# Performance work log

Measured on AMD Instinct MI355X. Metric: run time of the kernel, lower is better.

The kernel has to match this reference:

```python
import jax, jax.numpy as jnp
import numpy as np

N_LAYERS = 24  # number of recurrent applications of the shared HashLinear


def setup_inputs() -> dict:
    key = jax.random.key(0)
    ks = jax.random.split(key, 9)
    B, D_IN, N, N_OUT = 1024, 784, 4096, 10
    s_in = 1.0 / np.sqrt(D_IN)
    s_h = 1.0 / np.sqrt(N)
    x = jax.random.normal(ks[0], (B, D_IN), jnp.float32)
    # nn.Linear(prod(input_dim), 2*n_units)
    W_in = jax.random.uniform(ks[1], (2 * N, D_IN), jnp.float32, -s_in, s_in)
    b_in = jax.random.uniform(ks[2], (2 * N,), jnp.float32, -s_in, s_in)
    # HashLinear(n_units, n_units, period=1, 'hash'): learnable +/-1 context key + shared linear
    key_sp = jnp.where(jax.random.bernoulli(ks[3], 0.5, (1, N)), 1.0, -1.0).astype(jnp.float32)
    W_sp = jax.random.uniform(ks[4], (N, N), jnp.float32, -s_h, s_h)
    b_sp = jax.random.uniform(ks[5], (N,), jnp.float32, -s_h, s_h)
    # HashLinear(n_units, 10, period=1, 'hash')
    key_f = jnp.where(jax.random.bernoulli(ks[6], 0.5, (1, N)), 1.0, -1.0).astype(jnp.float32)
    W_f = jax.random.uniform(ks[7], (N_OUT, N), jnp.float32, -s_h, s_h)
    b_f = jax.random.uniform(ks[8], (N_OUT,), jnp.float32, -s_h, s_h)
    return {"x": x, "W_in": W_in, "b_in": b_in, "key_sp": key_sp, "W_sp": W_sp,
            "b_sp": b_sp, "key_f": key_f, "W_f": W_f, "b_f": b_f, "time": 0}


def _hash_linear(xa, xb, o, W, b):
    # Superposition HashLinear: same shared weight applied to both streams,
    # each modulated by the +/-1 context key o ([n_in]).
    ya = (xa * o) @ W.T + b
    yb = (xb * o) @ W.T + b
    return ya, yb


def reference(x, W_in, b_in, key_sp, W_sp, b_sp, key_f, W_f, b_f, time):
    N = W_sp.shape[0]
    r = x @ W_in.T + b_in                 # [B, 2N]
    r_a, r_b = r[:, :N], r[:, N:]         # torch.split(r, n_units, 1)
    pre0 = r_a
    r_a, r_b = jax.nn.relu(r_a), jax.nn.relu(r_b)
    o = key_sp[time % key_sp.shape[0]]    # period=1, time=0 in the module

    def step(carry, _):
        a, b2 = carry
        ya, yb = _hash_linear(a, b2, o, W_sp, b_sp)
        return (jax.nn.relu(ya), jax.nn.relu(yb)), ya  # collect preactivation r_a

    (r_a, r_b), pres = jax.lax.scan(step, (r_a, r_b), None, length=N_LAYERS)
    of = key_f[time % key_f.shape[0]]
    out_a, out_b = _hash_linear(r_a, r_b, of, W_f, b_f)  # [B,10], [B,10]
    preactivations = jnp.concatenate([pre0[None], pres], axis=0)  # [N_LAYERS+1, B, N]
    return (out_a, out_b, preactivations)
```

## Files before the change

kernel.cpp:

```cpp
#include <hip/hip_runtime.h>
#include <hip/hip_bf16.h>
#include <stdint.h>

typedef __bf16 bf16x8 __attribute__((ext_vector_type(8)));
typedef float  f32x4  __attribute__((ext_vector_type(4)));
typedef unsigned short ushort8v __attribute__((ext_vector_type(8)));

#define NH      4096
#define MB      1024
#define M2      2048
#define DIN     784
#define KPAD    832
#define N_IN    8192
#define NLAYERS 24
#define NOUT    10

#define ASL     (128 * 64)
#define SLOT    (2 * ASL)

__device__ __forceinline__ unsigned short f2bf(float x) {
  union { float f; unsigned u; } v; v.f = x;
  unsigned r = v.u + 0x7FFFu + ((v.u >> 16) & 1u);
  return (unsigned short)(r >> 16);
}
__device__ __forceinline__ float bf2f(unsigned short u) {
  union { unsigned u; float f; } v; v.u = ((unsigned)u) << 16; return v.f;
}

__device__ __forceinline__ void async16(const void* g, void* l) {
  __builtin_amdgcn_global_load_lds(
      (const __attribute__((address_space(1))) void*)g,
      (__attribute__((address_space(3))) void*)l, 16, 0, 0);
}

__global__ void k_conv_wsp(const float* __restrict__ W, const float* __restrict__ o,
                           unsigned short* __restrict__ out) {
  size_t i = ((size_t)blockIdx.x * blockDim.x + threadIdx.x) * 4;
  if (i >= (size_t)NH * NH) return;
  float4 w = *reinterpret_cast<const float4*>(W + i);
  int k = (int)(i & (NH - 1));
  float4 ov = *reinterpret_cast<const float4*>(o + k);
  ushort4 r;
  r.x = f2bf(w.x * ov.x); r.y = f2bf(w.y * ov.y);
  r.z = f2bf(w.z * ov.z); r.w = f2bf(w.w * ov.w);
  *reinterpret_cast<ushort4*>(out + i) = r;
}

__global__ void k_conv_pad2(const float* __restrict__ Win, const float* __restrict__ x,
                            unsigned short* __restrict__ Win_bf,
                            unsigned short* __restrict__ X_bf) {
  size_t i = (size_t)blockIdx.x * blockDim.x + threadIdx.x;
  if (i >= (size_t)(N_IN + MB) * KPAD) return;
  int r = (int)(i / KPAD), c = (int)(i % KPAD);
  if (r < N_IN) Win_bf[i] = (c < DIN) ? f2bf(Win[(size_t)r * DIN + c]) : (unsigned short)0;
  else {
    int rr = r - N_IN;
    X_bf[(size_t)rr * KPAD + c] = (c < DIN) ? f2bf(x[(size_t)rr * DIN + c]) : (unsigned short)0;
  }
}

__device__ __forceinline__ void gemm_core(
    const unsigned short* __restrict__ Ag, const unsigned short* __restrict__ Bg,
    int K, int bm, int bn, unsigned short* lds, f32x4 acc[4][4])
{
  const int t    = threadIdx.x;
  const int lane = t & 63;
  const int wave = t >> 6;
  const int wm   = wave >> 1;
  const int wn   = wave & 1;
  const int l15  = lane & 15;
  const int lkb  = (lane >> 4) * 16;

  const int srow = t >> 3;
  const int sb   = ((t & 7) * 16) ^ ((srow & 7) << 4);
  const unsigned aG0 = (unsigned)((bm + srow) * K + (sb >> 1));
  const unsigned bG0 = (unsigned)((bn + srow) * K + (sb >> 1));

  auto STAGE = [&](int bufIdx, int k0) {
    unsigned short* s = lds + bufIdx * SLOT;
#pragma unroll
    for (int j = 0; j < 4; ++j)
      async16(Ag + aG0 + (unsigned)(j * 32 * K + k0), s + t * 8 + j * 2048);
#pragma unroll
    for (int j = 0; j < 4; ++j)
      async16(Bg + bG0 + (unsigned)(j * 32 * K + k0), s + ASL + t * 8 + j * 2048);
  };

  int aRd[2][4], bRd[2][4];
#pragma unroll
  for (int kk = 0; kk < 2; ++kk)
#pragma unroll
    for (int i = 0; i < 4; ++i) {
      const int ra = wm * 64 + i * 16 + l15;
      aRd[kk][i] = (ra * 128 + ((kk * 64 + lkb) ^ ((ra & 7) << 4))) >> 1;
      const int rb = wn * 64 + i * 16 + l15;
      bRd[kk][i] = (rb * 128 + ((kk * 64 + lkb) ^ ((rb & 7) << 4))) >> 1;
    }

  const int nt = K >> 6;
  STAGE(0, 0);
  asm volatile("s_waitcnt vmcnt(0)" ::: "memory");
  __builtin_amdgcn_s_barrier();

  int buf = 0;
  for (int kt = 0; kt < nt; ++kt) {
    if (kt + 1 < nt) STAGE(buf ^ 1, (kt + 1) << 6);
    const unsigned short* base = lds + buf * SLOT;
    __builtin_amdgcn_s_setprio(1);
#pragma unroll
    for (int kk = 0; kk < 2; ++kk) {
      bf16x8 a[4], b[4];
#pragma unroll
      for (int i = 0; i < 4; ++i) a[i] = *reinterpret_cast<const bf16x8*>(base + aRd[kk][i]);
#pragma unroll
      for (int i = 0; i < 4; ++i) b[i] = *reinterpret_cast<const bf16x8*>(base + ASL + bRd[kk][i]);
#pragma unroll
      for (int mi = 0; mi < 4; ++mi)
#pragma unroll
        for (int ni = 0; ni < 4; ++ni)
          acc[mi][ni] = __builtin_amdgcn_mfma_f32_16x16x32_bf16(a[mi], b[ni], acc[mi][ni], 0, 0, 0);
    }
    __builtin_amdgcn_s_setprio(0);
    if (kt + 1 < nt) {
      asm volatile("s_waitcnt vmcnt(0)" ::: "memory");
      __builtin_amdgcn_s_barrier();
    }
    buf ^= 1;
  }
}

__global__ __launch_bounds__(256, 2) void k_gemm_layer(
    const unsigned short* __restrict__ A, const unsigned short* __restrict__ W,
    const float* __restrict__ bias, float* __restrict__ preact,
    unsigned short* __restrict__ Anext)
{
  __shared__ __align__(16) unsigned short lds[2 * SLOT];
  const int bid = blockIdx.x;
  const int xcd = bid & 7;
  const int idx = bid >> 3;
  const int bm  = (idx >> 2) * 128;
  const int bn  = (xcd * 4 + (idx & 3)) * 128;
  f32x4 acc[4][4] = {};
  gemm_core(A, W, NH, bm, bn, lds, acc);

  const int lane = threadIdx.x & 63;
  const int wave = threadIdx.x >> 6;
  const int wm = (wave >> 1) * 64, wn = (wave & 1) * 64;
  const int l15 = lane & 15;
#pragma unroll
  for (int mi = 0; mi < 4; ++mi) {
    const int gm0 = bm + wm + mi * 16 + (lane >> 4) * 4;
#pragma unroll
    for (int ni = 0; ni < 4; ++ni) {
      const int gn = bn + wn + ni * 16 + l15;
      const float bv = bias[gn];
#pragma unroll
      for (int r = 0; r < 4; ++r) {
        const int gm = gm0 + r;
        const float y = acc[mi][ni][r] + bv;
        if (gm < MB) preact[(size_t)gm * NH + gn] = y;
        Anext[(size_t)gm * NH + gn] = f2bf(y > 0.f ? y : 0.f);
      }
    }
  }
}

__global__ __launch_bounds__(256, 2) void k_gemm_in(
    const unsigned short* __restrict__ X, const unsigned short* __restrict__ W,
    const float* __restrict__ bias, float* __restrict__ preact0,
    unsigned short* __restrict__ A0)
{
  __shared__ __align__(16) unsigned short lds[2 * SLOT];
  const int bid = blockIdx.x;
  const int xcd = bid & 7;
  const int idx = bid >> 3;
  const int bm  = (idx >> 3) * 128;
  const int bn  = (xcd * 8 + (idx & 7)) * 128;
  f32x4 acc[4][4] = {};
  gemm_core(X, W, KPAD, bm, bn, lds, acc);

  const int lane = threadIdx.x & 63;
  const int wave = threadIdx.x >> 6;
  const int wm = (wave >> 1) * 64, wn = (wave & 1) * 64;
  const int l15 = lane & 15;
#pragma unroll
  for (int mi = 0; mi < 4; ++mi) {
    const int gm0 = bm + wm + mi * 16 + (lane >> 4) * 4;
#pragma unroll
    for (int ni = 0; ni < 4; ++ni) {
      const int gn = bn + wn + ni * 16 + l15;
      const float bv = bias[gn];
#pragma unroll
      for (int r = 0; r < 4; ++r) {
        const int gm = gm0 + r;
        const float y = acc[mi][ni][r] + bv;
        const unsigned short rl = f2bf(y > 0.f ? y : 0.f);
        if (gn < NH) {
          preact0[(size_t)gm * NH + gn] = y;
          A0[(size_t)gm * NH + gn] = rl;
        } else {
          A0[(size_t)(MB + gm) * NH + (gn - NH)] = rl;
        }
      }
    }
  }
}

__global__ __launch_bounds__(256) void k_final(
    const unsigned short* __restrict__ A, const float* __restrict__ Wf,
    const float* __restrict__ of, const float* __restrict__ bf_,
    float* __restrict__ out)
{
  __shared__ float red[4][NOUT];
  const int t = threadIdx.x;
  for (int rr = 0; rr < 8; ++rr) {
    const int m = blockIdx.x * 8 + rr;
    float accj[NOUT];
#pragma unroll
    for (int j = 0; j < NOUT; ++j) accj[j] = 0.f;
    for (int k0 = t * 8; k0 < NH; k0 += 256 * 8) {
      const ushort8v av = *reinterpret_cast<const ushort8v*>(A + (size_t)m * NH + k0);
      const float4 o0 = *reinterpret_cast<const float4*>(of + k0);
      const float4 o1 = *reinterpret_cast<const float4*>(of + k0 + 4);
      float a[8];
      a[0] = bf2f(av[0]) * o0.x; a[1] = bf2f(av[1]) * o0.y;
      a[2] = bf2f(av[2]) * o0.z; a[3] = bf2f(av[3]) * o0.w;
      a[4] = bf2f(av[4]) * o1.x; a[5] = bf2f(av[5]) * o1.y;
      a[6] = bf2f(av[6]) * o1.z; a[7] = bf2f(av[7]) * o1.w;
#pragma unroll
      for (int j = 0; j < NOUT; ++j) {
        const float4 w0 = *reinterpret_cast<const float4*>(Wf + (size_t)j * NH + k0);
        const float4 w1 = *reinterpret_cast<const float4*>(Wf + (size_t)j * NH + k0 + 4);
        accj[j] += a[0]*w0.x + a[1]*w0.y + a[2]*w0.z + a[3]*w0.w
                 + a[4]*w1.x + a[5]*w1.y + a[6]*w1.z + a[7]*w1.w;
      }
    }
#pragma unroll
    for (int j = 0; j < NOUT; ++j) {
      float v = accj[j];
      for (int off = 32; off > 0; off >>= 1) v += __shfl_down(v, off);
      if ((t & 63) == 0) red[t >> 6][j] = v;
    }
    __syncthreads();
    if (t < NOUT)
      out[(size_t)m * NOUT + t] = red[0][t] + red[1][t] + red[2][t] + red[3][t] + bf_[t];
    __syncthreads();
  }
}

extern "C" void kernel_launch(void* const* d_in, const int* in_sizes, int n_in,
                              void* d_out, int out_size, void* d_ws, size_t ws_size,
                              hipStream_t stream) {
  const float* x     = (const float*)d_in[0];
  const float* W_in  = (const float*)d_in[1];
  const float* b_in  = (const float*)d_in[2];
  const float* keysp = (const float*)d_in[3];
  const float* W_sp  = (const float*)d_in[4];
  const float* b_sp  = (const float*)d_in[5];
  const float* keyf  = (const float*)d_in[6];
  const float* W_f   = (const float*)d_in[7];
  const float* b_f   = (const float*)d_in[8];

  float* out    = (float*)d_out;
  float* preact = out + (size_t)2 * MB * NOUT;

  char* ws = (char*)d_ws;
  unsigned short* Wsp_bf = (unsigned short*)ws;  ws += (size_t)NH * NH * 2;
  unsigned short* A0     = (unsigned short*)ws;  ws += (size_t)M2 * NH * 2;
  unsigned short* A1     = (unsigned short*)ws;  ws += (size_t)M2 * NH * 2;
  unsigned short* Win_bf = (unsigned short*)ws;  ws += (size_t)N_IN * KPAD * 2;
  unsigned short* X_bf   = (unsigned short*)ws;  ws += (size_t)MB * KPAD * 2;

  k_conv_wsp<<<(NH * (size_t)NH / 4 + 255) / 256, 256, 0, stream>>>(W_sp, keysp, Wsp_bf);
  k_conv_pad2<<<((size_t)(N_IN + MB) * KPAD + 255) / 256, 256, 0, stream>>>(
      W_in, x, Win_bf, X_bf);

  k_gemm_in<<<512, 256, 0, stream>>>(X_bf, Win_bf, b_in, preact, A0);

  unsigned short* Ain = A0;
  unsigned short* Aout = A1;
  for (int tlay = 0; tlay < NLAYERS; ++tlay) {
    float* pre = preact + (size_t)(tlay + 1) * MB * NH;
    k_gemm_layer<<<512, 256, 0, stream>>>(Ain, Wsp_bf, b_sp, pre, Aout);
    unsigned short* tmp = Ain; Ain = Aout; Aout = tmp;
  }

  k_final<<<M2 / 8, 256, 0, stream>>>(Ain, W_f, keyf, b_f, out);
}
```

Baseline: 1.618 ms.

## Switch GEMM mainloop to BK=32 with 5-slot LDS ring and 3-deep prefetch

Replaces the double-buffered K=64 tile pipeline with a five-slot ring of K=32 tiles. Three stages are kept in flight, and partial vmcnt waits let the loop block only on the oldest stage, not drain all loads every iteration. The LDS swizzle is redesigned for the 64-byte row pitch. The goal is to hide global-load latency better behind MFMA work. In exchange there are twice as many barriers per K, the MFMA batch per iteration is smaller, and LDS usage per block is larger.

Measured after the change: 1.942 ms. 1.2x slower.

```diff
diff --git a/kernel.cpp b/kernel.cpp
--- a/kernel.cpp
+++ b/kernel.cpp
@@ -15,8 +15,8 @@
 #define NLAYERS 24
 #define NOUT    10
 
-#define ASL     (128 * 64)
-#define SLOT    (2 * ASL)
+#define ASL32   (128 * 32)
+#define SLOT    (2 * ASL32)
 
 __device__ __forceinline__ unsigned short f2bf(float x) {
   union { float f; unsigned u; } v; v.f = x;
@@ -25,6 +25,9 @@
 }
 __device__ __forceinline__ float bf2f(unsigned short u) {
   union { unsigned u; float f; } v; v.u = ((unsigned)u) << 16; return v.f;
+}
+__device__ __forceinline__ int swz5(int row) {
+  return (row & 3) ^ ((row >> 2) & 3);
 }
 
 __device__ __forceinline__ void async16(const void* g, void* l) {
@@ -69,63 +72,65 @@
   const int wm   = wave >> 1;
   const int wn   = wave & 1;
   const int l15  = lane & 15;
-  const int lkb  = (lane >> 4) * 16;
-
-  const int srow = t >> 3;
-  const int sb   = ((t & 7) * 16) ^ ((srow & 7) << 4);
-  const unsigned aG0 = (unsigned)((bm + srow) * K + (sb >> 1));
-  const unsigned bG0 = (unsigned)((bn + srow) * K + (sb >> 1));
-
-  auto STAGE = [&](int bufIdx, int k0) {
-    unsigned short* s = lds + bufIdx * SLOT;
-#pragma unroll
-    for (int j = 0; j < 4; ++j)
-      async16(Ag + aG0 + (unsigned)(j * 32 * K + k0), s + t * 8 + j * 2048);
-#pragma unroll
-    for (int j = 0; j < 4; ++j)
-      async16(Bg + bG0 + (unsigned)(j * 32 * K + k0), s + ASL + t * 8 + j * 2048);
+  const int sk   = lane >> 4;
+
+  unsigned aGo[2], bGo[2]; int dL[2];
+#pragma unroll
+  for (int j = 0; j < 2; ++j) {
+    const int c   = j * 256 + t;
+    const int row = c >> 2;
+    const int cs  = (c & 3) ^ swz5(row);
+    dL[j]  = c * 8;
+    aGo[j] = (unsigned)((bm + row) * K + cs * 8);
+    bGo[j] = (unsigned)((bn + row) * K + cs * 8);
+  }
+
+  auto STAGE = [&](int slotIdx, int k0) {
+    unsigned short* s = lds + slotIdx * SLOT;
+#pragma unroll
+    for (int j = 0; j < 2; ++j) {
+      async16(Ag + aGo[j] + (unsigned)k0, s + dL[j]);
+      async16(Bg + bGo[j] + (unsigned)k0, s + ASL32 + dL[j]);
+    }
   };
 
-  int aRd[2][4], bRd[2][4];
-#pragma unroll
-  for (int kk = 0; kk < 2; ++kk)
-#pragma unroll
-    for (int i = 0; i < 4; ++i) {
-      const int ra = wm * 64 + i * 16 + l15;
-      aRd[kk][i] = (ra * 128 + ((kk * 64 + lkb) ^ ((ra & 7) << 4))) >> 1;
-      const int rb = wn * 64 + i * 16 + l15;
-      bRd[kk][i] = (rb * 128 + ((kk * 64 + lkb) ^ ((rb & 7) << 4))) >> 1;
-    }
-
-  const int nt = K >> 6;
+  int aRd[4], bRd[4];
+#pragma unroll
+  for (int i = 0; i < 4; ++i) {
+    const int ra = wm * 64 + i * 16 + l15;
+    aRd[i] = ra * 32 + ((sk ^ swz5(ra)) * 8);
+    const int rb = wn * 64 + i * 16 + l15;
+    bRd[i] = rb * 32 + ((sk ^ swz5(rb)) * 8);
+  }
+
+  const int nt = K >> 5;
   STAGE(0, 0);
-  asm volatile("s_waitcnt vmcnt(0)" ::: "memory");
-  __builtin_amdgcn_s_barrier();
-
-  int buf = 0;
+  if (nt > 1) STAGE(1, 32);
+  if (nt > 2) STAGE(2, 64);
+
+  int s0 = 0, s3 = 3;
   for (int kt = 0; kt < nt; ++kt) {
-    if (kt + 1 < nt) STAGE(buf ^ 1, (kt + 1) << 6);
-    const unsigned short* base = lds + buf * SLOT;
+    const int rem = nt - 1 - kt;
+    if (rem >= 2)      asm volatile("s_waitcnt vmcnt(8)" ::: "memory");
+    else if (rem == 1) asm volatile("s_waitcnt vmcnt(4)" ::: "memory");
+    else               asm volatile("s_waitcnt vmcnt(0)" ::: "memory");
+    __builtin_amdgcn_s_barrier();
+    if (kt + 3 < nt) STAGE(s3, (kt + 3) << 5);
+    const unsigned short* base = lds + s0 * SLOT;
     __builtin_amdgcn_s_setprio(1);
-#pragma unroll
-    for (int kk = 0; kk < 2; ++kk) {
-      bf16x8 a[4], b[4];
-#pragma unroll
-      for (int i = 0; i < 4; ++i) a[i] = *reinterpret_cast<const bf16x8*>(base + aRd[kk][i]);
-#pragma unroll
-      for (int i = 0; i < 4; ++i) b[i] = *reinterpret_cast<const bf16x8*>(base + ASL + bRd[kk][i]);
-#pragma unroll
-      for (int mi = 0; mi < 4; ++mi)
-#pragma unroll
-        for (int ni = 0; ni < 4; ++ni)
-          acc[mi][ni] = __builtin_amdgcn_mfma_f32_16x16x32_bf16(a[mi], b[ni], acc[mi][ni], 0, 0, 0);
-    }
+    bf16x8 a[4], b[4];
+#pragma unroll
+    for (int i = 0; i < 4; ++i) a[i] = *reinterpret_cast<const bf16x8*>(base + aRd[i]);
+#pragma unroll
+    for (int i = 0; i < 4; ++i) b[i] = *reinterpret_cast<const bf16x8*>(base + ASL32 + bRd[i]);
+#pragma unroll
+    for (int mi = 0; mi < 4; ++mi)
+#pragma unroll
+      for (int ni = 0; ni < 4; ++ni)
+        acc[mi][ni] = __builtin_amdgcn_mfma_f32_16x16x32_bf16(a[mi], b[ni], acc[mi][ni], 0, 0, 0);
     __builtin_amdgcn_s_setprio(0);
-    if (kt + 1 < nt) {
-      asm volatile("s_waitcnt vmcnt(0)" ::: "memory");
-      __builtin_amdgcn_s_barrier();
-    }
-    buf ^= 1;
+    s0 = (s0 == 4) ? 0 : s0 + 1;
+    s3 = (s3 == 4) ? 0 : s3 + 1;
   }
 }
 
@@ -134,7 +139,7 @@
     const float* __restrict__ bias, float* __restrict__ preact,
     unsigned short* __restrict__ Anext)
 {
-  __shared__ __align__(16) unsigned short lds[2 * SLOT];
+  __shared__ __align__(16) unsigned short lds[5 * SLOT];
   const int bid = blockIdx.x;
   const int xcd = bid & 7;
   const int idx = bid >> 3;
@@ -170,7 +175,7 @@
     const float* __restrict__ bias, float* __restrict__ preact0,
     unsigned short* __restrict__ A0)
 {
-  __shared__ __align__(16) unsigned short lds[2 * SLOT];
+  __shared__ __align__(16) unsigned short lds[5 * SLOT];
   const int bid = blockIdx.x;
   const int xcd = bid & 7;
   const int idx = bid >> 3;
```
